# Kernel tuning notes

Measured on AMD Instinct MI355X. Metric: run time of the kernel, lower is better.

The kernel has to match this reference:

```python
import jax, jax.numpy as jnp
import numpy as np

N, C, D = 131072, 1024, 128

def setup_inputs() -> dict:
    key = jax.random.key(0)
    kx, kw = jax.random.split(key)
    x = jax.random.normal(kx, (N, D), dtype=jnp.float32)
    prototypes = jax.random.normal(kw, (C, D), dtype=jnp.float32)
    return {"x": x, "prototypes": prototypes}

def reference(x, prototypes):
    # Pairwise squared Euclidean distance: dist[n, c] = sum_d (x[n,d] - w[c,d])^2
    x_sq = jnp.sum(x * x, axis=-1, keepdims=True)            # [N, 1]
    w_sq = jnp.sum(prototypes * prototypes, axis=-1)          # [C]
    cross = jnp.einsum('nd,cd->nc', x, prototypes)            # [N, C]
    return x_sq + w_sq[None, :] - 2.0 * cross                 # [N, C]
```

## Files before the change

### kernel.cpp

```cpp
#include <hip/hip_runtime.h>
#include <cstdint>
#include <cstddef>

#define D_DIM 128

typedef __attribute__((ext_vector_type(8))) __bf16 bf16x8;
typedef __attribute__((ext_vector_type(4))) float f32x4;

__device__ __forceinline__ unsigned short f2bf(float f) {
    unsigned u = __builtin_bit_cast(unsigned, f);
    u += 0x7FFFu + ((u >> 16) & 1u);
    return (unsigned short)(u >> 16);
}
__device__ __forceinline__ float bf2f(unsigned short h) {
    unsigned u = ((unsigned)h) << 16;
    return __builtin_bit_cast(float, u);
}

__global__ __launch_bounds__(256) void prep_kernel(
    const float* __restrict__ x, const float* __restrict__ w,
    unsigned short* __restrict__ xb, unsigned short* __restrict__ wb,
    float* __restrict__ xsq, float* __restrict__ wsq,
    int n_rows_x, int n_rows_w)
{
    const int wave = threadIdx.x >> 6;
    const int lane = threadIdx.x & 63;
    int row = blockIdx.x * 4 + wave;
    const float* src; unsigned short* dst; float* nrm; int r;
    if (row < n_rows_x) { src = x; dst = xb; nrm = xsq; r = row; }
    else {
        r = row - n_rows_x;
        if (r >= n_rows_w) return;
        src = w; dst = wb; nrm = wsq;
    }
    const float2* srow = reinterpret_cast<const float2*>(src + (size_t)r * D_DIM);
    float2 v = srow[lane];
    unsigned short b0 = f2bf(v.x), b1 = f2bf(v.y);
    float f0 = bf2f(b0), f1 = bf2f(b1);
    unsigned pack = (unsigned)b0 | ((unsigned)b1 << 16);
    reinterpret_cast<unsigned*>(dst + (size_t)r * D_DIM)[lane] = pack;
    float s = f0 * f0 + f1 * f1;
    #pragma unroll
    for (int off = 32; off > 0; off >>= 1) s += __shfl_xor(s, off, 64);
    if (lane == 0) nrm[r] = s;
}

__global__ __launch_bounds__(256, 2) void rbf_gemm(
    const unsigned short* __restrict__ xb, const unsigned short* __restrict__ wb,
    const float* __restrict__ xsq, const float* __restrict__ wsq,
    float* __restrict__ out, int C_total)
{
    __shared__ __align__(16) unsigned short As[128 * 128];
    __shared__ __align__(16) unsigned short Bs[128 * 128];

    const int tid    = threadIdx.x;
    const int wave   = tid >> 6;
    const int lane   = tid & 63;
    const int lane16 = lane & 15;
    const int quad   = lane >> 4;

    const long c0 = (long)blockIdx.x * 128;
    const long m0 = (long)blockIdx.y * 128;

    {
        const unsigned short* gA = xb + (size_t)m0 * D_DIM;
        const unsigned short* gB = wb + (size_t)c0 * D_DIM;
        #pragma unroll
        for (int i = 0; i < 8; ++i) {
            const int chunk = wave * 8 + i;
            const unsigned short* ga = gA + chunk * 512 + lane * 8;
            __builtin_amdgcn_global_load_lds(
                (const __attribute__((address_space(1))) unsigned*)ga,
                (__attribute__((address_space(3))) unsigned*)(As + chunk * 512),
                16, 0, 0);
        }
        #pragma unroll
        for (int i = 0; i < 8; ++i) {
            const int chunk = wave * 8 + i;
            const unsigned short* gb = gB + chunk * 512 + lane * 8;
            __builtin_amdgcn_global_load_lds(
                (const __attribute__((address_space(1))) unsigned*)gb,
                (__attribute__((address_space(3))) unsigned*)(Bs + chunk * 512),
                16, 0, 0);
        }
    }
    __syncthreads();

    const int wm = (wave & 1) * 64;
    const int wc = (wave >> 1) * 64;

    f32x4 acc[4][4];
    #pragma unroll
    for (int i = 0; i < 4; ++i)
        #pragma unroll
        for (int j = 0; j < 4; ++j)
            acc[i][j] = (f32x4){0.f, 0.f, 0.f, 0.f};

    #pragma unroll
    for (int kk = 0; kk < 128; kk += 32) {
        bf16x8 a[4], b[4];
        #pragma unroll
        for (int mt = 0; mt < 4; ++mt)
            a[mt] = *reinterpret_cast<const bf16x8*>(
                &As[(wm + mt * 16 + lane16) * 128 + kk + quad * 8]);
        #pragma unroll
        for (int ct = 0; ct < 4; ++ct)
            b[ct] = *reinterpret_cast<const bf16x8*>(
                &Bs[(wc + ct * 16 + lane16) * 128 + kk + quad * 8]);
        #pragma unroll
        for (int mt = 0; mt < 4; ++mt)
            #pragma unroll
            for (int ct = 0; ct < 4; ++ct)
                acc[mt][ct] = __builtin_amdgcn_mfma_f32_16x16x32_bf16(
                    a[mt], b[ct], acc[mt][ct], 0, 0, 0);
    }

    float wsqv[4];
    #pragma unroll
    for (int ct = 0; ct < 4; ++ct)
        wsqv[ct] = wsq[c0 + wc + ct * 16 + lane16];

    #pragma unroll
    for (int mt = 0; mt < 4; ++mt) {
        const long rbase = m0 + wm + mt * 16 + quad * 4;
        float xs[4];
        #pragma unroll
        for (int i = 0; i < 4; ++i) xs[i] = xsq[rbase + i];
        #pragma unroll
        for (int ct = 0; ct < 4; ++ct) {
            const long col = c0 + wc + ct * 16 + lane16;
            #pragma unroll
            for (int i = 0; i < 4; ++i) {
                out[(rbase + i) * (long)C_total + col] =
                    xs[i] + wsqv[ct] - 2.0f * acc[mt][ct][i];
            }
        }
    }
}

extern "C" void kernel_launch(void* const* d_in, const int* in_sizes, int n_in,
                              void* d_out, int out_size, void* d_ws, size_t ws_size,
                              hipStream_t stream) {
    const float* x = (const float*)d_in[0];
    const float* w = (const float*)d_in[1];
    float* out = (float*)d_out;

    const int N = in_sizes[0] / D_DIM;
    const int C = in_sizes[1] / D_DIM;

    unsigned short* xb = (unsigned short*)d_ws;
    unsigned short* wb = xb + (size_t)N * D_DIM;
    float* xsq = (float*)(wb + (size_t)C * D_DIM);
    float* wsq = xsq + N;

    const int rows = N + C;
    prep_kernel<<<(rows + 3) / 4, 256, 0, stream>>>(x, w, xb, wb, xsq, wsq, N, C);

    dim3 grid(C / 128, N / 128);
    rbf_gemm<<<grid, 256, 0, stream>>>(xb, wb, xsq, wsq, out, C);
}
```

Baseline: 612.9 us.

## Load MFMA operands directly from global and stage epilogue through LDS for vector stores

Drops the A/B shared-memory staging and the block barrier, so each wave reads its bf16 operand fragments straight from global memory (relying on cache reuse between waves). The epilogue now writes accumulators into a padded per-wave LDS transpose buffer, so each lane can emit 16-byte float4 stores of contiguous columns instead of scalar strided stores. It also removes the occupancy hint from launch bounds. The output write of N*C floats dominates traffic, so wider coalesced stores target the main cost, at the price of redundant global operand loads.

```diff
diff --git a/kernel.cpp b/kernel.cpp
--- a/kernel.cpp
+++ b/kernel.cpp
@@ -45,13 +45,14 @@
     if (lane == 0) nrm[r] = s;
 }
 
-__global__ __launch_bounds__(256, 2) void rbf_gemm(
+#define TLDS_STRIDE 68
+
+__global__ __launch_bounds__(256) void rbf_gemm(
     const unsigned short* __restrict__ xb, const unsigned short* __restrict__ wb,
     const float* __restrict__ xsq, const float* __restrict__ wsq,
     float* __restrict__ out, int C_total)
 {
-    __shared__ __align__(16) unsigned short As[128 * 128];
-    __shared__ __align__(16) unsigned short Bs[128 * 128];
+    __shared__ float tlds[4][16 * TLDS_STRIDE];
 
     const int tid    = threadIdx.x;
     const int wave   = tid >> 6;
@@ -62,32 +63,11 @@
     const long c0 = (long)blockIdx.x * 128;
     const long m0 = (long)blockIdx.y * 128;
 
-    {
-        const unsigned short* gA = xb + (size_t)m0 * D_DIM;
-        const unsigned short* gB = wb + (size_t)c0 * D_DIM;
-        #pragma unroll
-        for (int i = 0; i < 8; ++i) {
-            const int chunk = wave * 8 + i;
-            const unsigned short* ga = gA + chunk * 512 + lane * 8;
-            __builtin_amdgcn_global_load_lds(
-                (const __attribute__((address_space(1))) unsigned*)ga,
-                (__attribute__((address_space(3))) unsigned*)(As + chunk * 512),
-                16, 0, 0);
-        }
-        #pragma unroll
-        for (int i = 0; i < 8; ++i) {
-            const int chunk = wave * 8 + i;
-            const unsigned short* gb = gB + chunk * 512 + lane * 8;
-            __builtin_amdgcn_global_load_lds(
-                (const __attribute__((address_space(1))) unsigned*)gb,
-                (__attribute__((address_space(3))) unsigned*)(Bs + chunk * 512),
-                16, 0, 0);
-        }
-    }
-    __syncthreads();
-
     const int wm = (wave & 1) * 64;
     const int wc = (wave >> 1) * 64;
+
+    const unsigned short* aBase = xb + ((size_t)(m0 + wm) + lane16) * D_DIM + quad * 8;
+    const unsigned short* bBase = wb + ((size_t)(c0 + wc) + lane16) * D_DIM + quad * 8;
 
     f32x4 acc[4][4];
     #pragma unroll
@@ -101,12 +81,10 @@
         bf16x8 a[4], b[4];
         #pragma unroll
         for (int mt = 0; mt < 4; ++mt)
-            a[mt] = *reinterpret_cast<const bf16x8*>(
-                &As[(wm + mt * 16 + lane16) * 128 + kk + quad * 8]);
+            a[mt] = *reinterpret_cast<const bf16x8*>(aBase + (size_t)mt * 16 * D_DIM + kk);
         #pragma unroll
         for (int ct = 0; ct < 4; ++ct)
-            b[ct] = *reinterpret_cast<const bf16x8*>(
-                &Bs[(wc + ct * 16 + lane16) * 128 + kk + quad * 8]);
+            b[ct] = *reinterpret_cast<const bf16x8*>(bBase + (size_t)ct * 16 * D_DIM + kk);
         #pragma unroll
         for (int mt = 0; mt < 4; ++mt)
             #pragma unroll
@@ -115,25 +93,29 @@
                     a[mt], b[ct], acc[mt][ct], 0, 0, 0);
     }
 
-    float wsqv[4];
-    #pragma unroll
-    for (int ct = 0; ct < 4; ++ct)
-        wsqv[ct] = wsq[c0 + wc + ct * 16 + lane16];
+    const f32x4 wq = *reinterpret_cast<const f32x4*>(&wsq[c0 + wc + lane16 * 4]);
+    float* buf = tlds[wave];
 
     #pragma unroll
     for (int mt = 0; mt < 4; ++mt) {
-        const long rbase = m0 + wm + mt * 16 + quad * 4;
-        float xs[4];
         #pragma unroll
-        for (int i = 0; i < 4; ++i) xs[i] = xsq[rbase + i];
+        for (int ct = 0; ct < 4; ++ct)
+            #pragma unroll
+            for (int i = 0; i < 4; ++i)
+                buf[(quad * 4 + i) * TLDS_STRIDE + ct * 16 + lane16] = acc[mt][ct][i];
+
         #pragma unroll
-        for (int ct = 0; ct < 4; ++ct) {
-            const long col = c0 + wc + ct * 16 + lane16;
+        for (int j = 0; j < 4; ++j) {
+            const int row_local = j * 4 + quad;
+            f32x4 v = *reinterpret_cast<const f32x4*>(
+                &buf[row_local * TLDS_STRIDE + lane16 * 4]);
+            const long row = m0 + wm + mt * 16 + row_local;
+            const float xs = xsq[row];
+            f32x4 r;
             #pragma unroll
-            for (int i = 0; i < 4; ++i) {
-                out[(rbase + i) * (long)C_total + col] =
-                    xs[i] + wsqv[ct] - 2.0f * acc[mt][ct][i];
-            }
+            for (int k = 0; k < 4; ++k)
+                r[k] = xs + wq[k] - 2.0f * v[k];
+            *reinterpret_cast<f32x4*>(&out[row * (long)C_total + c0 + wc + lane16 * 4]) = r;
         }
     }
 }
```

Measured after the change: 668.1 us. 9.0% more time.
